# Performance work log

Hardware: AMD Instinct MI355X
Metric: run time of the kernel (lower is better)

## Reference

```python
import jax, jax.numpy as jnp
import numpy as np


def _fft_feats(x):
    # x: [B, 3, H, W] float32
    B, C, H, W = x.shape
    gray = 0.299 * x[:, 0] + 0.587 * x[:, 1] + 0.114 * x[:, 2]  # [B,H,W]
    mag = jnp.abs(jnp.fft.fftshift(jnp.fft.fft2(gray), axes=(-2, -1))) + 1e-8
    mag = mag / (mag.max(axis=(-2, -1), keepdims=True) + 1e-8)
    m = mag.reshape(B, -1)
    n = m.shape[1]
    mean = m.mean(axis=1)
    std = jnp.clip(jnp.std(m, axis=1, ddof=1), 1e-8, None)  # torch unbiased std
    mx = m.max(axis=1)
    mn = m.min(axis=1)
    gt_mean = (m > mean[:, None]).astype(jnp.float32).mean(axis=1)
    # torch.median returns the lower of the two middle values for even n
    med = jnp.sort(m, axis=1)[:, (n - 1) // 2]
    q1 = mag[:, : H // 4].mean(axis=(1, 2))
    q2 = mag[:, H // 4 : H // 2].mean(axis=(1, 2))
    q3 = mag[:, H // 2 : 3 * H // 4].mean(axis=(1, 2))
    q4 = mag[:, 3 * H // 4 :].mean(axis=(1, 2))
    gt_half = (m > 0.5).astype(jnp.float32).mean(axis=1)
    gt_tenth = (m > 0.1).astype(jnp.float32).mean(axis=1)
    feats = jnp.stack([mean, std, mx, mn, gt_mean, med, q1, q2, q3, q4, gt_half, gt_tenth], axis=1)
    return jnp.clip(feats, -10.0, 10.0)  # [B,12]


def _bn(h, gamma, beta):
    # BatchNorm1d, training-mode forward (batch statistics, biased var), eps=1e-5
    mu = h.mean(axis=0)
    var = h.var(axis=0)
    return gamma * (h - mu) / jnp.sqrt(var + 1e-5) + beta


def _mlp(f, W1, b1, g1, be1, W2, b2, g2, be2, W3, b3):
    h = jax.nn.relu(_bn(f @ W1 + b1, g1, be1))  # Dropout(0.1) treated as identity (eval)
    h = jax.nn.relu(_bn(h @ W2 + b2, g2, be2))
    return h @ W3 + b3


def setup_inputs() -> dict:
    key = jax.random.key(0)
    ks = jax.random.split(key, 8)
    B, H, W = 64, 512, 512
    D = 512  # output_dim
    x = jax.random.normal(ks[0], (B, 3, H, W), dtype=jnp.float32)
    W1 = jax.random.normal(ks[1], (12, 64), dtype=jnp.float32) * 0.2
    b1 = jnp.zeros((64,), jnp.float32)
    g1 = jnp.ones((64,), jnp.float32)
    be1 = jnp.zeros((64,), jnp.float32)
    W2 = jax.random.normal(ks[2], (64, 128), dtype=jnp.float32) * 0.1
    b2 = jnp.zeros((128,), jnp.float32)
    g2 = jnp.ones((128,), jnp.float32)
    be2 = jnp.zeros((128,), jnp.float32)
    W3 = jax.random.normal(ks[3], (128, D), dtype=jnp.float32) * 0.08
    b3 = jnp.zeros((D,), jnp.float32)
    return {"x": x, "W1": W1, "b1": b1, "g1": g1, "be1": be1,
            "W2": W2, "b2": b2, "g2": g2, "be2": be2, "W3": W3, "b3": b3}


def reference(x, W1, b1, g1, be1, W2, b2, g2, be2, W3, b3):
    feats = _fft_feats(x)
    return _mlp(feats, W1, b1, g1, be1, W2, b2, g2, be2, W3, b3)
```

## Files before the change

### kernel.cpp

```cpp
#include <hip/hip_runtime.h>
#include <math.h>

#ifndef M_PI
#define M_PI 3.14159265358979323846
#endif

#define BB 64
#define HH 512
#define WW 512
#define NPIX (HH*WW)
#define MED_K 131072u
#define WS 260
#define BSTRIDE 264
#define SS 520

__device__ __forceinline__ float wredf(float v){
  #pragma unroll
  for (int o = 32; o > 0; o >>= 1) v += __shfl_down(v, o, 64);
  return v;
}
__device__ __forceinline__ float wred_min(float v){
  #pragma unroll
  for (int o = 32; o > 0; o >>= 1) v = fminf(v, __shfl_down(v, o, 64));
  return v;
}
__device__ __forceinline__ float wred_max(float v){
  #pragma unroll
  for (int o = 32; o > 0; o >>= 1) v = fmaxf(v, __shfl_down(v, o, 64));
  return v;
}
__device__ __forceinline__ unsigned wred_addu(unsigned v){
  #pragma unroll
  for (int o = 32; o > 0; o >>= 1) v += __shfl_down(v, o, 64);
  return v;
}
__device__ __forceinline__ float wred_add_all(float v){
  #pragma unroll
  for (int o = 32; o > 0; o >>= 1) v += __shfl_xor(v, o, 64);
  return v;
}

__global__ void init_kernel(float2* __restrict__ twg, unsigned* __restrict__ scal){
  int t = threadIdx.x;
  double a = -2.0 * M_PI * (double)t / 512.0;
  twg[t] = make_float2((float)cos(a), (float)sin(a));
  #pragma unroll
  for (int q = 0; q < 8; ++q){
    int w = t*8 + q;
    scal[w] = (w >= 64 && w < 128) ? 0xFFFFFFFFu : 0u;
  }
}

__device__ __forceinline__ void build_twid(float2* T, const float2* __restrict__ twg,
                                           int t, int nthr){
  for (int i = t; i < 510; i += nthr){
    int v = i + 2;
    int z = 31 - __clz(v);
    T[i] = twg[(v - (1 << z)) << (8 - z)];
  }
}

__device__ __forceinline__ void wave_fft512(float (&re)[8], float (&im)[8],
                                            const float2* T, int lane){
  {
    const int d = 1;
    bool hi = (lane & d) != 0;
    #pragma unroll
    for (int r = 0; r < 8; ++r){
      float pre = __shfl_xor(re[r], d, 64);
      float pim = __shfl_xor(im[r], d, 64);
      float ur = hi ? pre : re[r], ui = hi ? pim : im[r];
      float vr = hi ? re[r] : pre, vi = hi ? im[r] : pim;
      re[r] = hi ? ur - vr : ur + vr;
      im[r] = hi ? ui - vi : ui + vi;
    }
  }
  #pragma unroll
  for (int st = 2; st <= 6; ++st){
    const int d = 1 << (st - 1);
    float2 w = T[((1 << (st - 1)) - 2) + (lane & (d - 1))];
    bool hi = (lane & d) != 0;
    #pragma unroll
    for (int r = 0; r < 8; ++r){
      float pre = __shfl_xor(re[r], d, 64);
      float pim = __shfl_xor(im[r], d, 64);
      float ur = hi ? pre : re[r], ui = hi ? pim : im[r];
      float rr = hi ? re[r] : pre, ri = hi ? im[r] : pim;
      float vr = w.x*rr - w.y*ri;
      float vi = w.x*ri + w.y*rr;
      re[r] = hi ? ur - vr : ur + vr;
      im[r] = hi ? ui - vi : ui + vi;
    }
  }
  {
    float2 w = T[62 + lane];
    #pragma unroll
    for (int r = 0; r < 8; r += 2){
      float vr = w.x*re[r+1] - w.y*im[r+1];
      float vi = w.x*im[r+1] + w.y*re[r+1];
      float ur = re[r], ui = im[r];
      re[r]   = ur + vr; im[r]   = ui + vi;
      re[r+1] = ur - vr; im[r+1] = ui - vi;
    }
  }
  {
    float2 w0 = T[126 + lane];
    float2 w1 = T[190 + lane];
    #pragma unroll
    for (int rb = 0; rb < 8; rb += 4){
      {
        float vr = w0.x*re[rb+2] - w0.y*im[rb+2];
        float vi = w0.x*im[rb+2] + w0.y*re[rb+2];
        float ur = re[rb], ui = im[rb];
        re[rb]   = ur + vr; im[rb]   = ui + vi;
        re[rb+2] = ur - vr; im[rb+2] = ui - vi;
      }
      {
        float vr = w1.x*re[rb+3] - w1.y*im[rb+3];
        float vi = w1.x*im[rb+3] + w1.y*re[rb+3];
        float ur = re[rb+1], ui = im[rb+1];
        re[rb+1] = ur + vr; im[rb+1] = ui + vi;
        re[rb+3] = ur - vr; im[rb+3] = ui - vi;
      }
    }
  }
  {
    #pragma unroll
    for (int r = 0; r < 4; ++r){
      float2 w = T[254 + 64*r + lane];
      float vr = w.x*re[r+4] - w.y*im[r+4];
      float vi = w.x*im[r+4] + w.y*re[r+4];
      float ur = re[r], ui = im[r];
      re[r]   = ur + vr; im[r]   = ui + vi;
      re[r+4] = ur - vr; im[r+4] = ui - vi;
    }
  }
}

__global__ __launch_bounds__(256) void row_fft_kernel(const float* __restrict__ x,
                                                      const float2* __restrict__ twg,
                                                      float2* __restrict__ out){
  __shared__ float2 T[510];
  int t = threadIdx.x;
  build_twid(T, twg, t, 256);
  __syncthreads();
  int lane = t & 63, wv = t >> 6;
  int pair = blockIdx.x*4 + wv;
  int b = pair >> 8, hp = pair & 255;
  int K = (int)(__brev((unsigned)lane) >> 26);
  int c0 = K << 3;
  const float* p0 = x + (size_t)b*3*NPIX + (size_t)(2*hp)*WW + c0;
  const float* p1 = p0 + WW;
  float4 ra0 = *(const float4*)(p0);          float4 ra1 = *(const float4*)(p0+4);
  float4 ga0 = *(const float4*)(p0+NPIX);     float4 ga1 = *(const float4*)(p0+NPIX+4);
  float4 ba0 = *(const float4*)(p0+2*NPIX);   float4 ba1 = *(const float4*)(p0+2*NPIX+4);
  float4 rb0 = *(const float4*)(p1);          float4 rb1 = *(const float4*)(p1+4);
  float4 gb0 = *(const float4*)(p1+NPIX);     float4 gb1 = *(const float4*)(p1+NPIX+4);
  float4 bb0 = *(const float4*)(p1+2*NPIX);   float4 bb1 = *(const float4*)(p1+2*NPIX+4);
  float g0[8] = {0.299f*ra0.x + 0.587f*ga0.x + 0.114f*ba0.x,
                 0.299f*ra0.y + 0.587f*ga0.y + 0.114f*ba0.y,
                 0.299f*ra0.z + 0.587f*ga0.z + 0.114f*ba0.z,
                 0.299f*ra0.w + 0.587f*ga0.w + 0.114f*ba0.w,
                 0.299f*ra1.x + 0.587f*ga1.x + 0.114f*ba1.x,
                 0.299f*ra1.y + 0.587f*ga1.y + 0.114f*ba1.y,
                 0.299f*ra1.z + 0.587f*ga1.z + 0.114f*ba1.z,
                 0.299f*ra1.w + 0.587f*ga1.w + 0.114f*ba1.w};
  float g1[8] = {0.299f*rb0.x + 0.587f*gb0.x + 0.114f*bb0.x,
                 0.299f*rb0.y + 0.587f*gb0.y + 0.114f*bb0.y,
                 0.299f*rb0.z + 0.587f*gb0.z + 0.114f*bb0.z,
                 0.299f*rb0.w + 0.587f*gb0.w + 0.114f*bb0.w,
                 0.299f*rb1.x + 0.587f*gb1.x + 0.114f*bb1.x,
                 0.299f*rb1.y + 0.587f*gb1.y + 0.114f*bb1.y,
                 0.299f*rb1.z + 0.587f*gb1.z + 0.114f*bb1.z,
                 0.299f*rb1.w + 0.587f*gb1.w + 0.114f*bb1.w};
  float re[8], im[8];
  re[0]=g0[0]; re[4]=g0[1]; re[2]=g0[2]; re[6]=g0[3];
  re[1]=g0[4]; re[5]=g0[5]; re[3]=g0[6]; re[7]=g0[7];
  im[0]=g1[0]; im[4]=g1[1]; im[2]=g1[2]; im[6]=g1[3];
  im[1]=g1[4]; im[5]=g1[5]; im[3]=g1[6]; im[7]=g1[7];
  wave_fft512(re, im, T, lane);
  int row0 = (b << 9) + 2*hp;
  float2* o0 = out + (size_t)row0*BSTRIDE;
  float2* o1 = o0 + BSTRIDE;
  int srcl = (64 - lane) & 63;
  float p4r = __shfl(re[4], srcl, 64), p4i = __shfl(im[4], srcl, 64);
  float p5r = __shfl(re[5], srcl, 64), p5i = __shfl(im[5], srcl, 64);
  float p6r = __shfl(re[6], srcl, 64), p6i = __shfl(im[6], srcl, 64);
  float p7r = __shfl(re[7], srcl, 64), p7i = __shfl(im[7], srcl, 64);
  bool l0 = (lane == 0);
  {
    float zr = re[0], zi = im[0];
    float wr = l0 ? re[0] : p7r, wi = l0 ? im[0] : p7i;
    o0[lane] = make_float2(0.5f*(zr + wr), 0.5f*(zi - wi));
    o1[lane] = make_float2(0.5f*(zi + wi), 0.5f*(wr - zr));
  }
  {
    float zr = re[1], zi = im[1];
    float wr = l0 ? re[7] : p6r, wi = l0 ? im[7] : p6i;
    int k = lane + 64;
    o0[k] = make_float2(0.5f*(zr + wr), 0.5f*(zi - wi));
    o1[k] = make_float2(0.5f*(zi + wi), 0.5f*(wr - zr));
  }
  {
    float zr = re[2], zi = im[2];
    float wr = l0 ? re[6] : p5r, wi = l0 ? im[6] : p5i;
    int k = lane + 128;
    o0[k] = make_float2(0.5f*(zr + wr), 0.5f*(zi - wi));
    o1[k] = make_float2(0.5f*(zi + wi), 0.5f*(wr - zr));
  }
  {
    float zr = re[3], zi = im[3];
    float wr = l0 ? re[5] : p4r, wi = l0 ? im[5] : p4i;
    int k = lane + 192;
    o0[k] = make_float2(0.5f*(zr + wr), 0.5f*(zi - wi));
    o1[k] = make_float2(0.5f*(zi + wi), 0.5f*(wr - zr));
  }
  if (l0){
    float zr = re[4], zi = im[4];
    o0[256] = make_float2(zr, 0.f);
    o1[256] = make_float2(zi, 0.f);
  }
}

__global__ __launch_bounds__(512) void col_fft_kernel(const float2* __restrict__ in,
    const float2* __restrict__ twg,
    float* __restrict__ magc,
    unsigned* __restrict__ dmax, unsigned* __restrict__ dmin,
    double* __restrict__ sum, double* __restrict__ sumsq, double* __restrict__ qsum,
    unsigned* __restrict__ hist1)
{
  __shared__ float st_re[8*SS];
  __shared__ float st_im[8*SS];
  __shared__ float2 T[510];
  __shared__ unsigned hs[256];
  __shared__ float buff[8][8];
  int t = threadIdx.x;
  int lane = t & 63, wv = t >> 6;
  build_twid(T, twg, t, 512);
  if (t < 256) hs[t] = 0u;
  int b = blockIdx.x / 33;
  int j0 = (blockIdx.x % 33) << 3;
  const float2* base = in + (size_t)b * (size_t)(512*BSTRIDE);
  #pragma unroll
  for (int it = 0; it < 8; ++it){
    int idx = t + (it << 9);
    int e = idx >> 3, jj = idx & 7;
    float2 v = base[(size_t)e*BSTRIDE + j0 + jj];
    int se = e ^ (e >> 3);
    st_re[jj*SS + se] = v.x;
    st_im[jj*SS + se] = v.y;
  }
  __syncthreads();
  int j = j0 + wv;
  if (j <= 256){
    int K = (int)(__brev((unsigned)lane) >> 26);
    const int rv3[8] = {0,4,2,6,1,5,3,7};
    float re[8], im[8];
    #pragma unroll
    for (int r = 0; r < 8; ++r){
      int e = 8*K + rv3[r];
      int se = e ^ K;
      re[r] = st_re[wv*SS + se];
      im[r] = st_im[wv*SS + se];
    }
    wave_fft512(re, im, T, lane);
    unsigned wu = (j == 0 || j == 256) ? 1u : 2u;
    float* mo = magc + (size_t)b*(512*WS);
    float lsum=0.f, lsq=0.f, lq0=0.f, lq1=0.f, lq2=0.f, lq3=0.f;
    float lmn = 3.4e38f, lmx = 0.f;
    #pragma unroll
    for (int r = 0; r < 8; ++r){
      float m = sqrtf(re[r]*re[r] + im[r]*im[r]) + 1e-8f;
      int k = lane + 64*r;
      int si = (k + 256) & 511;
      mo[(size_t)si*WS + j] = m;
      float wm = (wu == 2u) ? m + m : m;
      lsum += wm;
      lsq = fmaf(wm, m, lsq);
      lmn = fminf(lmn, m); lmx = fmaxf(lmx, m);
      int qa = si >> 7;
      lq0 += (qa==0)?m:0.f; lq1 += (qa==1)?m:0.f; lq2 += (qa==2)?m:0.f; lq3 += (qa==3)?m:0.f;
      if (wu == 2u){
        int qb = si ? 3 - ((si-1) >> 7) : 0;
        lq0 += (qb==0)?m:0.f; lq1 += (qb==1)?m:0.f; lq2 += (qb==2)?m:0.f; lq3 += (qb==3)?m:0.f;
      }
      unsigned bin = __float_as_uint(m) >> 23;
      bool done = false;
      while (true){
        unsigned long long act = __ballot(!done);
        if (act == 0ull) break;
        int srcl = __ffsll(act) - 1;
        unsigned lbin = __shfl(bin, srcl, 64);
        bool match = (!done) && (bin == lbin);
        unsigned long long mb = __ballot(match);
        if (lane == srcl) atomicAdd(&hs[lbin], wu * (unsigned)__popcll(mb));
        done = done || match;
      }
    }
    float r0 = wredf(lsum), r1 = wredf(lsq);
    float r2 = wredf(lq0), r3 = wredf(lq1), r4 = wredf(lq2), r5 = wredf(lq3);
    float fmn = wred_min(lmn), fmx = wred_max(lmx);
    if (lane == 0){
      buff[0][wv]=r0; buff[1][wv]=r1; buff[2][wv]=r2;
      buff[3][wv]=r3; buff[4][wv]=r4; buff[5][wv]=r5;
      buff[6][wv]=fmn; buff[7][wv]=fmx;
    }
  }
  __syncthreads();
  int nact = 257 - j0; if (nact > 8) nact = 8;
  if (t == 0){
    double s0=0,s1=0,s2=0,s3=0,s4=0,s5=0; float mn=3.4e38f, mx=0.f;
    for (int i = 0; i < nact; ++i){
      s0+=(double)buff[0][i]; s1+=(double)buff[1][i]; s2+=(double)buff[2][i];
      s3+=(double)buff[3][i]; s4+=(double)buff[4][i]; s5+=(double)buff[5][i];
      mn=fminf(mn,buff[6][i]); mx=fmaxf(mx,buff[7][i]);
    }
    atomicAdd(sum + b, s0);
    atomicAdd(sumsq + b, s1);
    atomicAdd(qsum + b*4 + 0, s2);
    atomicAdd(qsum + b*4 + 1, s3);
    atomicAdd(qsum + b*4 + 2, s4);
    atomicAdd(qsum + b*4 + 3, s5);
    atomicMin(dmin + b, __float_as_uint(mn));
    atomicMax(dmax + b, __float_as_uint(mx));
  }
  unsigned* hb = hist1 + (size_t)b*256;
  if (t < 256){
    unsigned c = hs[t];
    if (c) atomicAdd(&hb[t], c);
  }
}

__global__ __launch_bounds__(256) void pass2_kernel(const float4* __restrict__ magc4,
    const unsigned* __restrict__ hist1, const double* __restrict__ sum,
    const unsigned* __restrict__ dmax,
    unsigned* __restrict__ hist2, unsigned* __restrict__ cnt_gtm,
    unsigned* __restrict__ cnt_half, unsigned* __restrict__ cnt_tenth)
{
  __shared__ unsigned h[16384];
  __shared__ unsigned part[256];
  __shared__ unsigned rb[3][8];
  __shared__ unsigned s_sel;
  int t = threadIdx.x, b = blockIdx.x;
  for (int i = t; i < 16384; i += 256) h[i] = 0;
  const unsigned* hb1 = hist1 + (size_t)b*256;
  part[t] = hb1[t];
  __syncthreads();
  if (t == 0){
    unsigned target = MED_K, cum = 0; int bin = 0;
    for (; bin < 256; ++bin){ if (cum + part[bin] >= target) break; cum += part[bin]; }
    s_sel = (unsigned)bin;
  }
  __syncthreads();
  unsigned s1 = s_sel;
  float meanf = (float)(sum[b] / (double)NPIX);
  float d = __uint_as_float(dmax[b]) + 1e-8f;
  float th = 0.5f*d, tl = 0.1f*d;
  const float4* p = magc4 + (size_t)b*(512*(WS/4)) + (size_t)blockIdx.y*128*(WS/4);
  unsigned lgm = 0, lh = 0, lt = 0;
  for (int idx = t; idx < 128*(WS/4); idx += 256){
    float4 v = p[idx];
    int k = idx % (WS/4);
    int jc0 = k*4;
    float a[4] = {v.x, v.y, v.z, v.w};
    #pragma unroll
    for (int q = 0; q < 4; ++q){
      int jc = jc0 + q;
      if (jc > 256) continue;
      unsigned w = (jc == 0 || jc == 256) ? 1u : 2u;
      float m = a[q];
      unsigned bits = __float_as_uint(m);
      if ((bits >> 23) == s1) atomicAdd(&h[(bits >> 9) & 0x3fffu], w);
      lgm += (m > meanf) ? w : 0u;
      lh  += (m > th) ? w : 0u;
      lt  += (m > tl) ? w : 0u;
    }
  }
  int lane = t & 63, wv = t >> 6;
  unsigned g0 = wred_addu(lgm), g1 = wred_addu(lh), g2 = wred_addu(lt);
  if (lane == 0){ rb[0][wv]=g0; rb[1][wv]=g1; rb[2][wv]=g2; }
  __syncthreads();
  if (t == 0){
    unsigned a0=0,a1=0,a2=0;
    for (int i = 0; i < 4; ++i){ a0+=rb[0][i]; a1+=rb[1][i]; a2+=rb[2][i]; }
    atomicAdd(cnt_gtm + b, a0);
    atomicAdd(cnt_half + b, a1);
    atomicAdd(cnt_tenth + b, a2);
  }
  unsigned* hb = hist2 + (size_t)b*16384;
  for (int i = t; i < 16384; i += 256){
    unsigned c = h[i];
    if (c) atomicAdd(&hb[i], c);
  }
}

__global__ __launch_bounds__(256) void scan2_feats_kernel(
    const unsigned* __restrict__ hist1, const unsigned* __restrict__ hist2,
    const unsigned* __restrict__ dmax, const unsigned* __restrict__ dmin,
    const double* __restrict__ sum, const double* __restrict__ sumsq,
    const double* __restrict__ qsum,
    const unsigned* __restrict__ cnt_half, const unsigned* __restrict__ cnt_tenth,
    const unsigned* __restrict__ cnt_gtmean,
    float* __restrict__ feats)
{
  int b = blockIdx.x, t = threadIdx.x;
  __shared__ unsigned part[256];
  __shared__ unsigned s_sel, s_rem;
  const unsigned* hb1 = hist1 + (size_t)b*256;
  part[t] = hb1[t];
  __syncthreads();
  if (t == 0){
    unsigned target = MED_K, cum = 0; int bin = 0;
    for (; bin < 256; ++bin){ if (cum + part[bin] >= target) break; cum += part[bin]; }
    s_sel = (unsigned)bin; s_rem = target - cum;
  }
  __syncthreads();
  const unsigned* hb2 = hist2 + (size_t)b*16384;
  {
    unsigned sp = 0;
    for (int i = 0; i < 64; ++i) sp += hb2[t*64 + i];
    part[t] = sp;
  }
  __syncthreads();
  if (t == 0){
    unsigned target = s_rem, cum = 0; int seg = 0;
    for (; seg < 256; ++seg){ if (cum + part[seg] >= target) break; cum += part[seg]; }
    unsigned r = target - cum;
    int bin = seg*64;
    for (;; ++bin){ unsigned c = hb2[bin]; if (c >= r) break; r -= c; }
    unsigned medbits = (s_sel << 23) | ((unsigned)bin << 9) | 256u;
    float maxv = __uint_as_float(dmax[b]);
    float dd_f = maxv + 1e-8f;
    double dd = (double)dd_f;
    double n = (double)NPIX;
    double sm = sum[b] / dd;
    double sq = sumsq[b] / (dd*dd);
    double mean = sm / n;
    double var = (sq - sm*sm/n) / (n - 1.0);
    if (var < 0.0) var = 0.0;
    float stdv = (float)sqrt(var);
    if (stdv < 1e-8f) stdv = 1e-8f;
    float f[12];
    f[0] = (float)mean;
    f[1] = stdv;
    f[2] = maxv / dd_f;
    f[3] = __uint_as_float(dmin[b]) / dd_f;
    f[4] = (float)((double)cnt_gtmean[b] / n);
    f[5] = __uint_as_float(medbits) / dd_f;
    f[6] = (float)(qsum[b*4+0] / dd * (1.0/65536.0));
    f[7] = (float)(qsum[b*4+1] / dd * (1.0/65536.0));
    f[8] = (float)(qsum[b*4+2] / dd * (1.0/65536.0));
    f[9] = (float)(qsum[b*4+3] / dd * (1.0/65536.0));
    f[10] = (float)((double)cnt_half[b] / n);
    f[11] = (float)((double)cnt_tenth[b] / n);
    #pragma unroll
    for (int i = 0; i < 12; ++i)
      feats[b*12 + i] = fminf(fmaxf(f[i], -10.f), 10.f);
  }
}

__global__ __launch_bounds__(64) void mlp1_kernel(const float* __restrict__ feats,
    const float* __restrict__ W1, const float* __restrict__ b1,
    const float* __restrict__ g1, const float* __restrict__ be1,
    float* __restrict__ h1t)
{
  int c = blockIdx.x, r = threadIdx.x;
  float acc = b1[c];
  #pragma unroll
  for (int k = 0; k < 12; ++k) acc += feats[r*12 + k] * W1[k*64 + c];
  float mu = wred_add_all(acc) * (1.f/BB);
  float dv = acc - mu;
  float var = wred_add_all(dv*dv) * (1.f/BB);
  float scv = g1[c] / sqrtf(var + 1e-5f);
  float v = dv*scv + be1[c];
  h1t[c*BB + r] = v > 0.f ? v : 0.f;
}

__global__ __launch_bounds__(64) void mlp2_kernel(const float* __restrict__ h1t,
    const float* __restrict__ W2, const float* __restrict__ b2,
    const float* __restrict__ g2, const float* __restrict__ be2,
    float* __restrict__ h2t)
{
  int c = blockIdx.x, r = threadIdx.x;
  float acc = b2[c];
  #pragma unroll 4
  for (int k = 0; k < 64; ++k) acc += h1t[k*BB + r] * W2[k*128 + c];
  float mu = wred_add_all(acc) * (1.f/BB);
  float dv = acc - mu;
  float var = wred_add_all(dv*dv) * (1.f/BB);
  float scv = g2[c] / sqrtf(var + 1e-5f);
  float v = dv*scv + be2[c];
  h2t[c*BB + r] = v > 0.f ? v : 0.f;
}

__global__ __launch_bounds__(256) void mlp3_kernel(const float* __restrict__ h2t,
    const float* __restrict__ W3, const float* __restrict__ b3,
    float* __restrict__ out)
{
  int r = threadIdx.x & 63;
  int w = threadIdx.x >> 6;
  int c = blockIdx.x*4 + w;
  float acc = b3[c];
  #pragma unroll 4
  for (int k = 0; k < 128; ++k) acc += h2t[k*BB + r] * W3[k*512 + c];
  out[r*512 + c] = acc;
}

extern "C" void kernel_launch(void* const* d_in, const int* in_sizes, int n_in,
                              void* d_out, int out_size, void* d_ws, size_t ws_size,
                              hipStream_t stream) {
  (void)in_sizes; (void)n_in; (void)out_size; (void)ws_size;
  const float* x   = (const float*)d_in[0];
  const float* W1  = (const float*)d_in[1];
  const float* b1  = (const float*)d_in[2];
  const float* g1  = (const float*)d_in[3];
  const float* be1 = (const float*)d_in[4];
  const float* W2  = (const float*)d_in[5];
  const float* b2  = (const float*)d_in[6];
  const float* g2  = (const float*)d_in[7];
  const float* be2 = (const float*)d_in[8];
  const float* W3  = (const float*)d_in[9];
  const float* b3  = (const float*)d_in[10];
  float* out = (float*)d_out;

  char* ws = (char*)d_ws;
  float2* bufc = (float2*)ws;
  float*  magc = (float*)(ws + 134217728);
  unsigned* hist1 = (unsigned*)(ws + 134217728 + 34078720);
  unsigned* hist2 = (unsigned*)(ws + 168296448 + 65536);
  char* sc = ws + 168361984 + 4194304;
  unsigned* dmax      = (unsigned*)(sc + 0);
  unsigned* dmin      = (unsigned*)(sc + 256);
  double*   sum       = (double*)(sc + 512);
  double*   sumsq     = (double*)(sc + 1024);
  double*   qsum      = (double*)(sc + 1536);
  unsigned* cnt_half  = (unsigned*)(sc + 3584);
  unsigned* cnt_tenth = (unsigned*)(sc + 3840);
  unsigned* cnt_gtm   = (unsigned*)(sc + 4096);
  float*    feats     = (float*)(sc + 5120);
  float*    h1t       = (float*)(sc + 8192);
  float*    h2t       = (float*)(sc + 8192 + 16384);
  float2*   twg       = (float2*)(sc + 8192 + 16384 + 32768);

  hipMemsetAsync(hist1, 0, 65536 + 4194304, stream);

  init_kernel<<<1, 256, 0, stream>>>(twg, (unsigned*)sc);
  row_fft_kernel<<<BB*64, 256, 0, stream>>>(x, twg, bufc);
  col_fft_kernel<<<BB*33, 512, 0, stream>>>(bufc, twg, magc, dmax, dmin, sum, sumsq, qsum, hist1);
  pass2_kernel<<<dim3(BB, 4), 256, 0, stream>>>((const float4*)magc, hist1, sum, dmax,
      hist2, cnt_gtm, cnt_half, cnt_tenth);
  scan2_feats_kernel<<<BB, 256, 0, stream>>>(hist1, hist2, dmax, dmin, sum, sumsq, qsum,
      cnt_half, cnt_tenth, cnt_gtm, feats);
  mlp1_kernel<<<64, 64, 0, stream>>>(feats, W1, b1, g1, be1, h1t);
  mlp2_kernel<<<128, 64, 0, stream>>>(h1t, W2, b2, g2, be2, h2t);
  mlp3_kernel<<<128, 256, 0, stream>>>(h2t, W3, b3, out);
}
```

Before: 460.8 us.

## Store magnitudes column-major, use per-wave shared histograms, coalesce row FFT loads

The column FFT kernel now writes the magnitude buffer column-contiguous (each column's 512 values stored together) instead of strided by row width, and pass2 reads columns in 65-column chunks with a per-column weight. The ballot-based histogram aggregation loop is replaced by direct shared-memory atomics into eight per-wave histograms, which are summed before the global flush. In the row FFT kernel each lane loads a contiguous chunk and bit-reversal reordering is done with cross-lane shuffles, replacing the bit-reversed load addresses. These changes target strided global stores, the serialized ballot loop, and uncoalesced loads, at the cost of extra shuffles and possible atomic contention within a wave.

New measurement: 441.7 us. 4.1% less time.

```diff
diff --git a/kernel.cpp b/kernel.cpp
--- a/kernel.cpp
+++ b/kernel.cpp
@@ -10,7 +10,7 @@
 #define WW 512
 #define NPIX (HH*WW)
 #define MED_K 131072u
-#define WS 260
+#define MAGB 131584
 #define BSTRIDE 264
 #define SS 520
 
@@ -147,8 +147,7 @@
   int lane = t & 63, wv = t >> 6;
   int pair = blockIdx.x*4 + wv;
   int b = pair >> 8, hp = pair & 255;
-  int K = (int)(__brev((unsigned)lane) >> 26);
-  int c0 = K << 3;
+  int c0 = lane << 3;
   const float* p0 = x + (size_t)b*3*NPIX + (size_t)(2*hp)*WW + c0;
   const float* p1 = p0 + WW;
   float4 ra0 = *(const float4*)(p0);          float4 ra1 = *(const float4*)(p0+4);
@@ -173,11 +172,16 @@
                  0.299f*rb1.y + 0.587f*gb1.y + 0.114f*bb1.y,
                  0.299f*rb1.z + 0.587f*gb1.z + 0.114f*bb1.z,
                  0.299f*rb1.w + 0.587f*gb1.w + 0.114f*bb1.w};
+  int src = (int)(__brev((unsigned)lane) >> 26);
   float re[8], im[8];
-  re[0]=g0[0]; re[4]=g0[1]; re[2]=g0[2]; re[6]=g0[3];
-  re[1]=g0[4]; re[5]=g0[5]; re[3]=g0[6]; re[7]=g0[7];
-  im[0]=g1[0]; im[4]=g1[1]; im[2]=g1[2]; im[6]=g1[3];
-  im[1]=g1[4]; im[5]=g1[5]; im[3]=g1[6]; im[7]=g1[7];
+  re[0] = __shfl(g0[0], src, 64); re[1] = __shfl(g0[4], src, 64);
+  re[2] = __shfl(g0[2], src, 64); re[3] = __shfl(g0[6], src, 64);
+  re[4] = __shfl(g0[1], src, 64); re[5] = __shfl(g0[5], src, 64);
+  re[6] = __shfl(g0[3], src, 64); re[7] = __shfl(g0[7], src, 64);
+  im[0] = __shfl(g1[0], src, 64); im[1] = __shfl(g1[4], src, 64);
+  im[2] = __shfl(g1[2], src, 64); im[3] = __shfl(g1[6], src, 64);
+  im[4] = __shfl(g1[1], src, 64); im[5] = __shfl(g1[5], src, 64);
+  im[6] = __shfl(g1[3], src, 64); im[7] = __shfl(g1[7], src, 64);
   wave_fft512(re, im, T, lane);
   int row0 = (b << 9) + 2*hp;
   float2* o0 = out + (size_t)row0*BSTRIDE;
@@ -232,12 +236,12 @@
   __shared__ float st_re[8*SS];
   __shared__ float st_im[8*SS];
   __shared__ float2 T[510];
-  __shared__ unsigned hs[256];
+  __shared__ unsigned h[8*256];
   __shared__ float buff[8][8];
   int t = threadIdx.x;
   int lane = t & 63, wv = t >> 6;
   build_twid(T, twg, t, 512);
-  if (t < 256) hs[t] = 0u;
+  for (int i = t; i < 2048; i += 512) h[i] = 0u;
   int b = blockIdx.x / 33;
   int j0 = (blockIdx.x % 33) << 3;
   const float2* base = in + (size_t)b * (size_t)(512*BSTRIDE);
@@ -265,7 +269,8 @@
     }
     wave_fft512(re, im, T, lane);
     unsigned wu = (j == 0 || j == 256) ? 1u : 2u;
-    float* mo = magc + (size_t)b*(512*WS);
+    float* mo = magc + (size_t)b*MAGB + (size_t)j*512;
+    unsigned* hw = h + (wv << 8);
     float lsum=0.f, lsq=0.f, lq0=0.f, lq1=0.f, lq2=0.f, lq3=0.f;
     float lmn = 3.4e38f, lmx = 0.f;
     #pragma unroll
@@ -273,28 +278,17 @@
       float m = sqrtf(re[r]*re[r] + im[r]*im[r]) + 1e-8f;
       int k = lane + 64*r;
       int si = (k + 256) & 511;
-      mo[(size_t)si*WS + j] = m;
+      mo[si] = m;
       float wm = (wu == 2u) ? m + m : m;
       lsum += wm;
       lsq = fmaf(wm, m, lsq);
       lmn = fminf(lmn, m); lmx = fmaxf(lmx, m);
+      atomicAdd(&hw[__float_as_uint(m) >> 23], wu);
       int qa = si >> 7;
       lq0 += (qa==0)?m:0.f; lq1 += (qa==1)?m:0.f; lq2 += (qa==2)?m:0.f; lq3 += (qa==3)?m:0.f;
       if (wu == 2u){
         int qb = si ? 3 - ((si-1) >> 7) : 0;
         lq0 += (qb==0)?m:0.f; lq1 += (qb==1)?m:0.f; lq2 += (qb==2)?m:0.f; lq3 += (qb==3)?m:0.f;
-      }
-      unsigned bin = __float_as_uint(m) >> 23;
-      bool done = false;
-      while (true){
-        unsigned long long act = __ballot(!done);
-        if (act == 0ull) break;
-        int srcl = __ffsll(act) - 1;
-        unsigned lbin = __shfl(bin, srcl, 64);
-        bool match = (!done) && (bin == lbin);
-        unsigned long long mb = __ballot(match);
-        if (lane == srcl) atomicAdd(&hs[lbin], wu * (unsigned)__popcll(mb));
-        done = done || match;
       }
     }
     float r0 = wredf(lsum), r1 = wredf(lsq);
@@ -326,7 +320,8 @@
   }
   unsigned* hb = hist1 + (size_t)b*256;
   if (t < 256){
-    unsigned c = hs[t];
+    unsigned c = h[t] + h[256+t] + h[512+t] + h[768+t]
+               + h[1024+t] + h[1280+t] + h[1536+t] + h[1792+t];
     if (c) atomicAdd(&hb[t], c);
   }
 }
@@ -339,7 +334,7 @@
 {
   __shared__ unsigned h[16384];
   __shared__ unsigned part[256];
-  __shared__ unsigned rb[3][8];
+  __shared__ unsigned rb[3][4];
   __shared__ unsigned s_sel;
   int t = threadIdx.x, b = blockIdx.x;
   for (int i = t; i < 16384; i += 256) h[i] = 0;
@@ -356,18 +351,18 @@
   float meanf = (float)(sum[b] / (double)NPIX);
   float d = __uint_as_float(dmax[b]) + 1e-8f;
   float th = 0.5f*d, tl = 0.1f*d;
-  const float4* p = magc4 + (size_t)b*(512*(WS/4)) + (size_t)blockIdx.y*128*(WS/4);
+  int c_lo = blockIdx.y * 65;
+  int ncols = 257 - c_lo; if (ncols > 65) ncols = 65;
+  const float4* p = magc4 + (size_t)b*(MAGB/4) + (size_t)c_lo*128;
   unsigned lgm = 0, lh = 0, lt = 0;
-  for (int idx = t; idx < 128*(WS/4); idx += 256){
+  int n4 = ncols * 128;
+  for (int idx = t; idx < n4; idx += 256){
     float4 v = p[idx];
-    int k = idx % (WS/4);
-    int jc0 = k*4;
+    int col = c_lo + (idx >> 7);
+    unsigned w = (col == 0 || col == 256) ? 1u : 2u;
     float a[4] = {v.x, v.y, v.z, v.w};
     #pragma unroll
     for (int q = 0; q < 4; ++q){
-      int jc = jc0 + q;
-      if (jc > 256) continue;
-      unsigned w = (jc == 0 || jc == 256) ? 1u : 2u;
       float m = a[q];
       unsigned bits = __float_as_uint(m);
       if ((bits >> 23) == s1) atomicAdd(&h[(bits >> 9) & 0x3fffu], w);
```
